# Kernel optimization log

Measured on AMD Instinct MI355X. Metric: run time of the kernel, lower is better.

## Reference

```python
import jax, jax.numpy as jnp
import numpy as np

OUT_FEATURES = 4096
IN_FEATURES = 4096


def _unpack_int4_symmetric(packed, n_values):
    # packed: uint8-valued int32 array; each byte holds two 4-bit values:
    # high nibble first, low nibble second (packing was (v0 << 4) | v1 with v in [0,15]=q+8)
    high = (packed >> 4) & 15
    low = packed & 15
    interleaved = jnp.stack([high, low], axis=-1).reshape(-1)[:n_values]
    # symmetric: quantized value q = nibble - 8, zero_point = 0
    return interleaved.astype(jnp.float32) - 8.0


def setup_inputs() -> dict:
    key = jax.random.key(0)
    k1, k2, k3, k4, k5 = jax.random.split(key, 5)
    x = jax.random.normal(k1, (4, 2048, IN_FEATURES), dtype=jnp.float32)
    packed_w = jax.random.randint(k2, (OUT_FEATURES * IN_FEATURES // 2,), 0, 256, dtype=jnp.int32)
    packed_b = jax.random.randint(k3, (OUT_FEATURES // 2,), 0, 256, dtype=jnp.int32)
    scale_w = jax.random.uniform(k4, (), dtype=jnp.float32) * 0.01 + 1e-4
    scale_b = jax.random.uniform(k5, (), dtype=jnp.float32) * 0.01 + 1e-4
    return {"x": x, "packed_w": packed_w, "packed_b": packed_b,
            "scale_w": scale_w, "scale_b": scale_b}


def reference(x, packed_w, packed_b, scale_w, scale_b):
    # dequantize weight: scale * (q - zero_point), zero_point = 0 (symmetric)
    qw = _unpack_int4_symmetric(packed_w, OUT_FEATURES * IN_FEATURES)
    W = (scale_w * qw).reshape(OUT_FEATURES, IN_FEATURES)  # [O, I]
    qb = _unpack_int4_symmetric(packed_b, OUT_FEATURES)
    b = scale_b * qb  # [O]
    # F.linear(x, W, b) = x @ W.T + b
    return jnp.einsum('bsi,oi->bso', x, W) + b
```

## Files before the change

### kernel.cpp

```cpp
#include <hip/hip_runtime.h>

#define M_DIM 8192
#define N_DIM 4096
#define K_DIM 4096

typedef _Float16 f16;
typedef _Float16 f16x8 __attribute__((ext_vector_type(8)));
typedef float f32x16 __attribute__((ext_vector_type(16)));

__device__ __forceinline__ void lds_async16(void* lds, const void* g) {
    __builtin_amdgcn_global_load_lds(
        (const __attribute__((address_space(1))) void*)(void*)g,
        (__attribute__((address_space(3))) void*)lds, 16, 0, 0);
}

__global__ __launch_bounds__(256) void cvt_x_kernel(const float* __restrict__ x, f16* __restrict__ xh) {
    size_t idx  = (size_t)blockIdx.x * 256 + threadIdx.x;
    size_t base = idx * 8;
    const float4* xp = (const float4*)(x + base);
    float4 v0 = xp[0], v1 = xp[1];
    f16x8 h;
    h[0] = (f16)v0.x; h[1] = (f16)v0.y; h[2] = (f16)v0.z; h[3] = (f16)v0.w;
    h[4] = (f16)v1.x; h[5] = (f16)v1.y; h[6] = (f16)v1.z; h[7] = (f16)v1.w;
    *(f16x8*)(xh + base) = h;
}

__global__ __launch_bounds__(256) void cvt_w_kernel(const int* __restrict__ pw, f16* __restrict__ wh) {
    size_t idx = (size_t)blockIdx.x * 256 + threadIdx.x;
    int4 v = ((const int4*)pw)[idx];
    f16x8 h;
    int a;
    a = v.x; h[0] = (f16)(((a >> 4) & 15) - 8); h[1] = (f16)((a & 15) - 8);
    a = v.y; h[2] = (f16)(((a >> 4) & 15) - 8); h[3] = (f16)((a & 15) - 8);
    a = v.z; h[4] = (f16)(((a >> 4) & 15) - 8); h[5] = (f16)((a & 15) - 8);
    a = v.w; h[6] = (f16)(((a >> 4) & 15) - 8); h[7] = (f16)((a & 15) - 8);
    *(f16x8*)(wh + idx * 8) = h;
}


#define PHASE(AC, BC, KK, STAGE_STMT, VM_STMT) do {                                              \
    const int h_   = (KK) >> 1;                                                                  \
    const int kc2_ = ((KK) & 1) * 2 + half;                                                      \
    f16x8 af0 = *(const f16x8*)&(AC)[h_ * 8192 + aoff[0] + ((kc2_ ^ axr[0]) << 3)];              \
    f16x8 af1 = *(const f16x8*)&(AC)[h_ * 8192 + aoff[1] + ((kc2_ ^ axr[1]) << 3)];              \
    f16x8 af2 = *(const f16x8*)&(AC)[h_ * 8192 + aoff[2] + ((kc2_ ^ axr[2]) << 3)];              \
    f16x8 af3 = *(const f16x8*)&(AC)[h_ * 8192 + aoff[3] + ((kc2_ ^ axr[3]) << 3)];              \
    f16x8 bf0 = *(const f16x8*)&(BC)[h_ * 8192 + boff[0] + ((kc2_ ^ bxr[0]) << 3)];              \
    f16x8 bf1 = *(const f16x8*)&(BC)[h_ * 8192 + boff[1] + ((kc2_ ^ bxr[1]) << 3)];              \
    STAGE_STMT;                                                                                  \
    __builtin_amdgcn_s_barrier();                                                                \
    asm volatile("s_waitcnt lgkmcnt(0)" ::: "memory");                                           \
    __builtin_amdgcn_sched_barrier(0);                                                           \
    __builtin_amdgcn_s_setprio(1);                                                               \
    acc[0][0] = __builtin_amdgcn_mfma_f32_32x32x16_f16(af0, bf0, acc[0][0], 0, 0, 0);            \
    acc[0][1] = __builtin_amdgcn_mfma_f32_32x32x16_f16(af0, bf1, acc[0][1], 0, 0, 0);            \
    acc[1][0] = __builtin_amdgcn_mfma_f32_32x32x16_f16(af1, bf0, acc[1][0], 0, 0, 0);            \
    acc[1][1] = __builtin_amdgcn_mfma_f32_32x32x16_f16(af1, bf1, acc[1][1], 0, 0, 0);            \
    acc[2][0] = __builtin_amdgcn_mfma_f32_32x32x16_f16(af2, bf0, acc[2][0], 0, 0, 0);            \
    acc[2][1] = __builtin_amdgcn_mfma_f32_32x32x16_f16(af2, bf1, acc[2][1], 0, 0, 0);            \
    acc[3][0] = __builtin_amdgcn_mfma_f32_32x32x16_f16(af3, bf0, acc[3][0], 0, 0, 0);            \
    acc[3][1] = __builtin_amdgcn_mfma_f32_32x32x16_f16(af3, bf1, acc[3][1], 0, 0, 0);            \
    __builtin_amdgcn_s_setprio(0);                                                               \
    VM_STMT;                                                                                     \
    __builtin_amdgcn_s_barrier();                                                                \
} while (0)

#define TILE_STEP(AC, BC, AN, BN, T) do {                                                        \
    const int kn_ = ((T) < 63) ? ((T) + 1) * 64 : 63 * 64;   \
    PHASE(AC, BC, 0,                                                                             \
          { lds_async16(&(AN)[dA0], aSrc[0] + kn_); lds_async16(&(AN)[dA1], aSrc[1] + kn_); },   \
          );                                                                                     \
    PHASE(AC, BC, 1,                                                                             \
          { lds_async16(&(BN)[dA0], bSrc[0] + kn_); lds_async16(&(BN)[dA1], bSrc[1] + kn_); },   \
          asm volatile("s_waitcnt vmcnt(4)" ::: "memory"));                                      \
    PHASE(AC, BC, 2,                                                                             \
          { lds_async16(&(AN)[8192 + dA0], aSrc[0] + kn_ + 32);                                  \
            lds_async16(&(AN)[8192 + dA1], aSrc[1] + kn_ + 32); },                               \
          );                                                                                     \
    PHASE(AC, BC, 3,                                                                             \
          { lds_async16(&(BN)[8192 + dA0], bSrc[0] + kn_ + 32);                                  \
            lds_async16(&(BN)[8192 + dA1], bSrc[1] + kn_ + 32); },                               \
          asm volatile("s_waitcnt vmcnt(4)" ::: "memory"));                                      \
} while (0)

__global__ __launch_bounds__(512, 2) void gemm_f16(const f16* __restrict__ A, const f16* __restrict__ B,
                                                   const int* __restrict__ pb,
                                                   const float* __restrict__ psw, const float* __restrict__ psb,
                                                   float* __restrict__ out) {
    __shared__ f16 As[2][16384];
    __shared__ f16 Bs[2][16384];

    const int tid  = threadIdx.x;
    const int wave = tid >> 6;
    const int lane = tid & 63;
    const int l32  = lane & 31;
    const int half = lane >> 5;
    const int wm   = wave >> 2;
    const int wn   = wave & 3;

    const int bid = blockIdx.x;
    const int swz = (bid & 7) * 64 + (bid >> 3);
    const int bx  = swz & 15;
    const int by  = swz >> 4;
    const int mbase = by * 256;
    const int nbase = bx * 256;

    const int rL   = ((lane >> 5) & 1) * 8 + ((lane >> 2) & 7);
    const int kswz = (((lane & 3) ^ ((lane >> 3) & 3))) * 8;
    const f16* aSrc[2]; const f16* bSrc[2];
#pragma unroll
    for (int j = 0; j < 2; j++) {
        aSrc[j] = A + (size_t)(mbase + j * 128 + wave * 16 + rL) * K_DIM + kswz;
        bSrc[j] = B + (size_t)(nbase + j * 128 + wave * 16 + rL) * K_DIM + kswz;
    }
    const int dA0 = wave * 512;
    const int dA1 = 4096 + wave * 512;

    int aoff[4], axr[4];
#pragma unroll
    for (int mt = 0; mt < 4; mt++) {
        int ra = wm * 128 + mt * 32 + l32;
        aoff[mt] = (ra >> 3) * 256 + (ra & 7) * 32;
        axr[mt]  = ((ra & 7) >> 1) & 3;
    }
    int boff[2], bxr[2];
#pragma unroll
    for (int nt = 0; nt < 2; nt++) {
        int rb = wn * 64 + nt * 32 + l32;
        boff[nt] = (rb >> 3) * 256 + (rb & 7) * 32;
        bxr[nt]  = ((rb & 7) >> 1) & 3;
    }

    f32x16 acc[4][2] = {};

    lds_async16(&As[0][dA0], aSrc[0]);
    lds_async16(&As[0][dA1], aSrc[1]);
    lds_async16(&Bs[0][dA0], bSrc[0]);
    lds_async16(&Bs[0][dA1], bSrc[1]);
    lds_async16(&As[0][8192 + dA0], aSrc[0] + 32);
    lds_async16(&As[0][8192 + dA1], aSrc[1] + 32);
    lds_async16(&Bs[0][8192 + dA0], bSrc[0] + 32);
    lds_async16(&Bs[0][8192 + dA1], bSrc[1] + 32);
    asm volatile("s_waitcnt vmcnt(4)" ::: "memory");
    __builtin_amdgcn_s_barrier();

#pragma unroll 1
    for (int t = 0; t < 64; t += 2) {
        TILE_STEP(As[0], Bs[0], As[1], Bs[1], t);
        TILE_STEP(As[1], Bs[1], As[0], Bs[0], t + 1);
    }

    asm volatile("s_waitcnt vmcnt(0)" ::: "memory");

    const float sw = *psw;
    const float sb = *psb;

#pragma unroll
    for (int nt = 0; nt < 2; nt++) {
        const int gcol = nbase + wn * 64 + nt * 32 + l32;
        const int p    = pb[gcol >> 1];
        const int nib  = (gcol & 1) ? (p & 15) : ((p >> 4) & 15);
        const float bias = sb * (float)(nib - 8);
#pragma unroll
        for (int mt = 0; mt < 4; mt++) {
            const int rbase = mbase + wm * 128 + mt * 32 + half * 4;
#pragma unroll
            for (int g = 0; g < 4; g++) {
                float* o = out + (size_t)(rbase + g * 8) * N_DIM + gcol;
#pragma unroll
                for (int r = 0; r < 4; r++)
                    o[(size_t)r * N_DIM] = sw * acc[mt][nt][g * 4 + r] + bias;
            }
        }
    }
}

__global__ __launch_bounds__(256) void gemm_fallback(const float* __restrict__ x, const int* __restrict__ pw,
                                                     const int* __restrict__ pb,
                                                     const float* __restrict__ psw, const float* __restrict__ psb,
                                                     float* __restrict__ out) {
    __shared__ float As[16][17];
    __shared__ float Bs[16][17];
    const int tx = threadIdx.x & 15, ty = threadIdx.x >> 4;
    const int row = blockIdx.y * 16 + ty;
    const int col = blockIdx.x * 16 + tx;
    float acc = 0.f;
    for (int k0 = 0; k0 < K_DIM; k0 += 16) {
        As[ty][tx] = x[(size_t)row * K_DIM + k0 + tx];
        const int nrow = blockIdx.x * 16 + ty;
        const int k = k0 + tx;
        const int p = pw[((size_t)nrow * K_DIM + k) >> 1];
        const int nib = (k & 1) ? (p & 15) : ((p >> 4) & 15);
        Bs[ty][tx] = (float)(nib - 8);
        __syncthreads();
#pragma unroll
        for (int kk = 0; kk < 16; kk++)
            acc += As[ty][kk] * Bs[tx][kk];
        __syncthreads();
    }
    const float sw = *psw, sb = *psb;
    const int p = pb[col >> 1];
    const int nib = (col & 1) ? (p & 15) : ((p >> 4) & 15);
    out[(size_t)row * N_DIM + col] = sw * acc + sb * (float)(nib - 8);
}

extern "C" void kernel_launch(void* const* d_in, const int* in_sizes, int n_in,
                              void* d_out, int out_size, void* d_ws, size_t ws_size,
                              hipStream_t stream) {
    (void)in_sizes; (void)n_in; (void)out_size;
    const float* x   = (const float*)d_in[0];
    const int*   pw  = (const int*)d_in[1];
    const int*   pb  = (const int*)d_in[2];
    const float* psw = (const float*)d_in[3];
    const float* psb = (const float*)d_in[4];
    float* out = (float*)d_out;

    const size_t xh_bytes = (size_t)M_DIM * K_DIM * sizeof(f16);
    const size_t wh_bytes = (size_t)N_DIM * K_DIM * sizeof(f16);

    if (ws_size >= xh_bytes + wh_bytes) {
        f16* xh = (f16*)d_ws;
        f16* wh = (f16*)((char*)d_ws + xh_bytes);
        cvt_x_kernel<<<(M_DIM * (size_t)K_DIM) / 8 / 256, 256, 0, stream>>>(x, xh);
        cvt_w_kernel<<<((size_t)N_DIM * K_DIM / 2) / 4 / 256, 256, 0, stream>>>(pw, wh);
        gemm_f16<<<dim3((M_DIM / 256) * (N_DIM / 256)), 512, 0, stream>>>(xh, wh, pb, psw, psb, out);
    } else {
        gemm_fallback<<<dim3(N_DIM / 16, M_DIM / 16), 256, 0, stream>>>(x, pw, pb, psw, psb, out);
    }
}
```

Baseline: 536.8 us.

## Replace fine-grained phased prefetch with whole-tile prefetch and single barrier per K step

Replaces the four-phase-per-tile schedule, which interleaved async global-to-LDS loads with MFMA groups and had two barriers per phase, with a simple loop. Each K step now issues all eight next-tile loads up front, runs all 32 MFMAs on the current buffer, then waits for all loads and does one barrier. This cuts barrier and waitcnt overhead. It loses the fine interleaving and the setprio hints, so load latency may be hidden less well. The prologue now waits for all loads instead of partial ones.

```diff
diff --git a/kernel.cpp b/kernel.cpp
--- a/kernel.cpp
+++ b/kernel.cpp
@@ -37,52 +37,6 @@
     *(f16x8*)(wh + idx * 8) = h;
 }
 
-
-#define PHASE(AC, BC, KK, STAGE_STMT, VM_STMT) do {                                              \
-    const int h_   = (KK) >> 1;                                                                  \
-    const int kc2_ = ((KK) & 1) * 2 + half;                                                      \
-    f16x8 af0 = *(const f16x8*)&(AC)[h_ * 8192 + aoff[0] + ((kc2_ ^ axr[0]) << 3)];              \
-    f16x8 af1 = *(const f16x8*)&(AC)[h_ * 8192 + aoff[1] + ((kc2_ ^ axr[1]) << 3)];              \
-    f16x8 af2 = *(const f16x8*)&(AC)[h_ * 8192 + aoff[2] + ((kc2_ ^ axr[2]) << 3)];              \
-    f16x8 af3 = *(const f16x8*)&(AC)[h_ * 8192 + aoff[3] + ((kc2_ ^ axr[3]) << 3)];              \
-    f16x8 bf0 = *(const f16x8*)&(BC)[h_ * 8192 + boff[0] + ((kc2_ ^ bxr[0]) << 3)];              \
-    f16x8 bf1 = *(const f16x8*)&(BC)[h_ * 8192 + boff[1] + ((kc2_ ^ bxr[1]) << 3)];              \
-    STAGE_STMT;                                                                                  \
-    __builtin_amdgcn_s_barrier();                                                                \
-    asm volatile("s_waitcnt lgkmcnt(0)" ::: "memory");                                           \
-    __builtin_amdgcn_sched_barrier(0);                                                           \
-    __builtin_amdgcn_s_setprio(1);                                                               \
-    acc[0][0] = __builtin_amdgcn_mfma_f32_32x32x16_f16(af0, bf0, acc[0][0], 0, 0, 0);            \
-    acc[0][1] = __builtin_amdgcn_mfma_f32_32x32x16_f16(af0, bf1, acc[0][1], 0, 0, 0);            \
-    acc[1][0] = __builtin_amdgcn_mfma_f32_32x32x16_f16(af1, bf0, acc[1][0], 0, 0, 0);            \
-    acc[1][1] = __builtin_amdgcn_mfma_f32_32x32x16_f16(af1, bf1, acc[1][1], 0, 0, 0);            \
-    acc[2][0] = __builtin_amdgcn_mfma_f32_32x32x16_f16(af2, bf0, acc[2][0], 0, 0, 0);            \
-    acc[2][1] = __builtin_amdgcn_mfma_f32_32x32x16_f16(af2, bf1, acc[2][1], 0, 0, 0);            \
-    acc[3][0] = __builtin_amdgcn_mfma_f32_32x32x16_f16(af3, bf0, acc[3][0], 0, 0, 0);            \
-    acc[3][1] = __builtin_amdgcn_mfma_f32_32x32x16_f16(af3, bf1, acc[3][1], 0, 0, 0);            \
-    __builtin_amdgcn_s_setprio(0);                                                               \
-    VM_STMT;                                                                                     \
-    __builtin_amdgcn_s_barrier();                                                                \
-} while (0)
-
-#define TILE_STEP(AC, BC, AN, BN, T) do {                                                        \
-    const int kn_ = ((T) < 63) ? ((T) + 1) * 64 : 63 * 64;   \
-    PHASE(AC, BC, 0,                                                                             \
-          { lds_async16(&(AN)[dA0], aSrc[0] + kn_); lds_async16(&(AN)[dA1], aSrc[1] + kn_); },   \
-          );                                                                                     \
-    PHASE(AC, BC, 1,                                                                             \
-          { lds_async16(&(BN)[dA0], bSrc[0] + kn_); lds_async16(&(BN)[dA1], bSrc[1] + kn_); },   \
-          asm volatile("s_waitcnt vmcnt(4)" ::: "memory"));                                      \
-    PHASE(AC, BC, 2,                                                                             \
-          { lds_async16(&(AN)[8192 + dA0], aSrc[0] + kn_ + 32);                                  \
-            lds_async16(&(AN)[8192 + dA1], aSrc[1] + kn_ + 32); },                               \
-          );                                                                                     \
-    PHASE(AC, BC, 3,                                                                             \
-          { lds_async16(&(BN)[8192 + dA0], bSrc[0] + kn_ + 32);                                  \
-            lds_async16(&(BN)[8192 + dA1], bSrc[1] + kn_ + 32); },                               \
-          asm volatile("s_waitcnt vmcnt(4)" ::: "memory"));                                      \
-} while (0)
-
 __global__ __launch_bounds__(512, 2) void gemm_f16(const f16* __restrict__ A, const f16* __restrict__ B,
                                                    const int* __restrict__ pb,
                                                    const float* __restrict__ psw, const float* __restrict__ psb,
@@ -141,16 +95,49 @@
     lds_async16(&As[0][8192 + dA1], aSrc[1] + 32);
     lds_async16(&Bs[0][8192 + dA0], bSrc[0] + 32);
     lds_async16(&Bs[0][8192 + dA1], bSrc[1] + 32);
-    asm volatile("s_waitcnt vmcnt(4)" ::: "memory");
+    asm volatile("s_waitcnt vmcnt(0)" ::: "memory");
     __builtin_amdgcn_s_barrier();
 
 #pragma unroll 1
-    for (int t = 0; t < 64; t += 2) {
-        TILE_STEP(As[0], Bs[0], As[1], Bs[1], t);
-        TILE_STEP(As[1], Bs[1], As[0], Bs[0], t + 1);
-    }
-
-    asm volatile("s_waitcnt vmcnt(0)" ::: "memory");
+    for (int t = 0; t < 64; ++t) {
+        const f16* Ac = As[t & 1];
+        const f16* Bc = Bs[t & 1];
+        f16* An = As[(t + 1) & 1];
+        f16* Bn = Bs[(t + 1) & 1];
+        const int kn = (t < 63 ? (t + 1) : 63) * 64;
+
+        lds_async16(&An[dA0], aSrc[0] + kn);
+        lds_async16(&An[dA1], aSrc[1] + kn);
+        lds_async16(&Bn[dA0], bSrc[0] + kn);
+        lds_async16(&Bn[dA1], bSrc[1] + kn);
+        lds_async16(&An[8192 + dA0], aSrc[0] + kn + 32);
+        lds_async16(&An[8192 + dA1], aSrc[1] + kn + 32);
+        lds_async16(&Bn[8192 + dA0], bSrc[0] + kn + 32);
+        lds_async16(&Bn[8192 + dA1], bSrc[1] + kn + 32);
+        __builtin_amdgcn_sched_barrier(0);
+
+#pragma unroll
+        for (int kk = 0; kk < 4; ++kk) {
+            const int h_   = kk >> 1;
+            const int kc2_ = (kk & 1) * 2 + half;
+            f16x8 af[4], bf[2];
+#pragma unroll
+            for (int mt = 0; mt < 4; mt++)
+                af[mt] = *(const f16x8*)&Ac[h_ * 8192 + aoff[mt] + ((kc2_ ^ axr[mt]) << 3)];
+#pragma unroll
+            for (int nt = 0; nt < 2; nt++)
+                bf[nt] = *(const f16x8*)&Bc[h_ * 8192 + boff[nt] + ((kc2_ ^ bxr[nt]) << 3)];
+#pragma unroll
+            for (int mt = 0; mt < 4; mt++)
+#pragma unroll
+                for (int nt = 0; nt < 2; nt++)
+                    acc[mt][nt] = __builtin_amdgcn_mfma_f32_32x32x16_f16(af[mt], bf[nt], acc[mt][nt], 0, 0, 0);
+        }
+
+        asm volatile("s_waitcnt vmcnt(0)" ::: "memory");
+        __builtin_amdgcn_s_barrier();
+        __builtin_amdgcn_sched_barrier(0);
+    }
 
     const float sw = *psw;
     const float sb = *psb;
```

Result: no change. 541.3 us (+0.8%).
